# Kernel optimization log

Hardware: AMD Instinct MI355X
Metric: run time of the kernel (lower is better)

The kernel has to match this reference:

```python
import jax, jax.numpy as jnp
import numpy as np

B, D, H, O, E = 1048576, 17, 8, 6, 4  # batch, input_dim, expert_hidden, output_dim, n_clusters
G1, G2 = 64, 32  # gating hidden dims


def setup_inputs() -> dict:
    key = jax.random.key(0)
    ks = jax.random.split(key, 14)
    def w(k, shape, fan_in):
        return (jax.random.normal(k, shape, jnp.float32) / jnp.sqrt(jnp.float32(fan_in)))
    return {
        "x": jax.random.normal(ks[0], (B, D), jnp.float32),
        # per-expert MLP params, stacked on leading expert axis E
        "eW1": w(ks[1], (E, D, H), D), "eb1": w(ks[2], (E, H), D),
        "eW2": w(ks[3], (E, H, H), H), "eb2": w(ks[4], (E, H), H),
        "eW3": w(ks[5], (E, H, O), H), "eb3": w(ks[6], (E, O), H),
        # gating classifier params
        "gW1": w(ks[7], (D, G1), D), "gb1": w(ks[8], (G1,), D),
        "gW2": w(ks[9], (G1, G2), G1), "gb2": w(ks[10], (G2,), G1),
        "gW3": w(ks[11], (G2, E), G2), "gb3": w(ks[12], (E,), G2),
    }


def reference(x, eW1, eb1, eW2, eb2, eW3, eb3, gW1, gb1, gW2, gb2, gW3, gb3):
    # gating network: 17 -> 64 -> 32 -> 4 logits
    h = jax.nn.relu(x @ gW1 + gb1)
    h = jax.nn.relu(h @ gW2 + gb2)
    gating_logits = h @ gW3 + gb3  # [B, E]
    selected = jnp.argmax(gating_logits, axis=1)  # [B] hard routing
    # all experts computed (as in the original), stacked over expert axis
    e = jax.nn.relu(jnp.einsum('bi,eih->beh', x, eW1) + eb1)   # [B, E, H]
    e = jax.nn.relu(jnp.einsum('beh,ehk->bek', e, eW2) + eb2)  # [B, E, H]
    eo = jnp.einsum('bek,eko->beo', e, eW3) + eb3              # [B, E, O]
    # gather the selected expert's output per sample
    predictions = jnp.take_along_axis(eo, selected[:, None, None], axis=1)[:, 0, :]  # [B, O]
    return predictions, gating_logits
```

## Files before the change

### kernel.cpp

```cpp
#include <hip/hip_runtime.h>

#define BTOT 1048576
#define D 17
#define H 8
#define OUT 6
#define E 4
#define G1 64
#define G2 32
#define CHUNKS 4
#define XSTR 20

typedef float f32x4 __attribute__((ext_vector_type(4)));
typedef float f32x2 __attribute__((ext_vector_type(2)));
typedef short s16x8 __attribute__((ext_vector_type(8)));
typedef unsigned int uint;
typedef unsigned short ushort_t;

union U4S8 { uint u[4]; s16x8 s; };

__device__ __forceinline__ uint bfr(uint u) {
    return (u + 0x7fffu + ((u >> 16) & 1u)) & 0xffff0000u;
}

__device__ __forceinline__ void split1(float v, uint &h, uint &m, uint &l) {
    uint hb = bfr(__float_as_uint(v));
    float r1 = v - __uint_as_float(hb);
    uint mb = bfr(__float_as_uint(r1));
    float r2 = r1 - __uint_as_float(mb);
    uint lb = bfr(__float_as_uint(r2));
    h = hb >> 16; m = mb >> 16; l = lb >> 16;
}

__device__ __forceinline__ void split_pair(float a, float b, uint &hp, uint &mp, uint &lp) {
    uint ha = bfr(__float_as_uint(a));
    uint hb = bfr(__float_as_uint(b));
    hp = (ha >> 16) | hb;
    float ra = a - __uint_as_float(ha);
    float rb = b - __uint_as_float(hb);
    uint ma = bfr(__float_as_uint(ra));
    uint mb = bfr(__float_as_uint(rb));
    mp = (ma >> 16) | mb;
    float sa = ra - __uint_as_float(ma);
    float sb = rb - __uint_as_float(mb);
    lp = (bfr(__float_as_uint(sa)) >> 16) | bfr(__float_as_uint(sb));
}

__device__ __forceinline__ void split8(f32x4 va, f32x4 vb, s16x8 &fh, s16x8 &fm, s16x8 &fl) {
    U4S8 Hh, Mm, Ll;
    split_pair(va.x, va.y, Hh.u[0], Mm.u[0], Ll.u[0]);
    split_pair(va.z, va.w, Hh.u[1], Mm.u[1], Ll.u[1]);
    split_pair(vb.x, vb.y, Hh.u[2], Mm.u[2], Ll.u[2]);
    split_pair(vb.z, vb.w, Hh.u[3], Mm.u[3], Ll.u[3]);
    fh = Hh.s; fm = Mm.s; fl = Ll.s;
}

#define MM6(dacc, ah, am, al, bh, bm, bl)                                        \
    dacc = __builtin_amdgcn_mfma_f32_16x16x32_bf16(al, bh, dacc, 0, 0, 0);       \
    dacc = __builtin_amdgcn_mfma_f32_16x16x32_bf16(am, bm, dacc, 0, 0, 0);       \
    dacc = __builtin_amdgcn_mfma_f32_16x16x32_bf16(ah, bl, dacc, 0, 0, 0);       \
    dacc = __builtin_amdgcn_mfma_f32_16x16x32_bf16(am, bh, dacc, 0, 0, 0);       \
    dacc = __builtin_amdgcn_mfma_f32_16x16x32_bf16(ah, bm, dacc, 0, 0, 0);       \
    dacc = __builtin_amdgcn_mfma_f32_16x16x32_bf16(ah, bh, dacc, 0, 0, 0);

#define WSTR 296

__global__ __launch_bounds__(256, 2) void hybrid_ruc_kernel(
    const float* __restrict__ x,
    const float* __restrict__ eW1, const float* __restrict__ eb1,
    const float* __restrict__ eW2, const float* __restrict__ eb2,
    const float* __restrict__ eW3, const float* __restrict__ eb3,
    const float* __restrict__ gW1, const float* __restrict__ gb1,
    const float* __restrict__ gW2, const float* __restrict__ gb2,
    const float* __restrict__ gW3, const float* __restrict__ gb3,
    float* __restrict__ out)
{
    __shared__ __align__(16) float    sxp[256 * XSTR];
    __shared__ __align__(16) ushort_t sW1[3][64 * 24];
    __shared__ __align__(16) ushort_t sW2[3][32 * 72];
    __shared__ __align__(16) ushort_t sW3[3][4 * 32];
    __shared__ __align__(16) float    sscr[4][1024];
    __shared__ __align__(16) float    swl[E * WSTR];

    const int tid = threadIdx.x;
    const int wv  = tid >> 6;
    const int ln  = tid & 63;
    const int g   = ln >> 4;
    const int nn  = ln & 15;
    float* scr = sscr[wv];

    for (int t = tid; t < 64 * 24; t += 256) {
        int n = t / 24, k = t % 24;
        float v = (k < D) ? gW1[k * G1 + n] : 0.0f;
        uint h, m, l; split1(v, h, m, l);
        sW1[0][t] = (ushort_t)h; sW1[1][t] = (ushort_t)m; sW1[2][t] = (ushort_t)l;
    }
    for (int t = tid; t < 32 * 64; t += 256) {
        int n = t >> 6, k = t & 63;
        uint h, m, l; split1(gW2[k * G2 + n], h, m, l);
        int a = n * 72 + k;
        sW2[0][a] = (ushort_t)h; sW2[1][a] = (ushort_t)m; sW2[2][a] = (ushort_t)l;
    }
    if (tid < 4 * 32) {
        int n = tid >> 5, k = tid & 31;
        uint h, m, l; split1(gW3[k * E + n], h, m, l);
        int a = n * 32 + k;
        sW3[0][a] = (ushort_t)h; sW3[1][a] = (ushort_t)m; sW3[2][a] = (ushort_t)l;
    }
    for (int t = tid; t < E * D * H; t += 256) {
        swl[(t / 136) * WSTR + (t % 136)] = eW1[t];
    }
    if (tid < E * H * H) {
        swl[(tid / 64) * WSTR + 144 + (tid % 64)] = eW2[tid];
    }
    if (tid < E * H * OUT) {
        int e = tid / 48, r = tid % 48, k = r / 6, o = r % 6;
        swl[e * WSTR + 216 + k * 8 + o] = eW3[tid];
    }
    if (tid < E * H) swl[(tid / 8) * WSTR + 136 + (tid % 8)] = eb1[tid];
    if (tid < E * H) swl[(tid / 8) * WSTR + 208 + (tid % 8)] = eb2[tid];
    if (tid < E * OUT) swl[(tid / 6) * WSTR + 280 + (tid % 6)] = eb3[tid];
    __syncthreads();

    float cb1[4], cb2[2], cb3;
    #pragma unroll
    for (int ct = 0; ct < 4; ++ct) cb1[ct] = gb1[ct * 16 + nn];
    cb2[0] = gb2[nn]; cb2[1] = gb2[16 + nn];
    cb3 = (nn < 4) ? gb3[nn] : 0.0f;

    const s16x8 z8 = {0, 0, 0, 0, 0, 0, 0, 0};
    s16x8 B1f[3][4];
    #pragma unroll
    for (int kd = 0; kd < 3; ++kd)
        #pragma unroll
        for (int ct = 0; ct < 4; ++ct)
            B1f[kd][ct] = (g <= 2) ? *(const s16x8*)(&sW1[kd][(ct * 16 + nn) * 24 + g * 8]) : z8;
    s16x8 B2f[3][2][2];
    #pragma unroll
    for (int kd = 0; kd < 3; ++kd)
        #pragma unroll
        for (int ct = 0; ct < 2; ++ct)
            #pragma unroll
            for (int kt = 0; kt < 2; ++kt)
                B2f[kd][ct][kt] = *(const s16x8*)(&sW2[kd][(ct * 16 + nn) * 72 + kt * 32 + g * 8]);
    s16x8 B3f[3];
    #pragma unroll
    for (int kd = 0; kd < 3; ++kd)
        B3f[kd] = (nn < 4) ? *(const s16x8*)(&sW3[kd][nn * 32 + g * 8]) : z8;

    #pragma unroll 1
    for (int c = 0; c < CHUNKS; ++c) {
        if (c) __syncthreads();
        const long long cbase = ((long long)blockIdx.x * CHUNKS + c) * 256;

        for (int t = tid; t < 256 * D; t += 256) {
            int s = t / D, k = t % D;
            sxp[s * XSTR + k] = x[cbase * D + t];
        }
        {
            int s = tid;
            sxp[s * XSTR + 17] = 0.0f;
            sxp[s * XSTR + 18] = 0.0f;
            sxp[s * XSTR + 19] = 0.0f;
        }
        __syncthreads();

        f32x4 Lg[4];
        const f32x4 z4 = {0.0f, 0.0f, 0.0f, 0.0f};
        #pragma unroll
        for (int rt = 0; rt < 4; ++rt) {
            const int srow = wv * 64 + rt * 16 + nn;
            f32x4 xa = (g <= 2) ? *(const f32x4*)(&sxp[srow * XSTR + g * 8]) : z4;
            f32x4 xb = (g <= 1) ? *(const f32x4*)(&sxp[srow * XSTR + g * 8 + 4]) : z4;
            s16x8 a1h, a1m, a1l; split8(xa, xb, a1h, a1m, a1l);

            #pragma unroll
            for (int ct = 0; ct < 4; ++ct) {
                f32x4 d = {cb1[ct], cb1[ct], cb1[ct], cb1[ct]};
                MM6(d, a1h, a1m, a1l, B1f[0][ct], B1f[1][ct], B1f[2][ct]);
                #pragma unroll
                for (int r = 0; r < 4; ++r) {
                    float hv = fmaxf(d[r], 0.0f);
                    int s = g * 4 + r, n = ct * 16 + nn;
                    scr[s * 64 + (((n >> 2) ^ (s & 15)) << 2) + (n & 3)] = hv;
                }
            }

            s16x8 a2h[2], a2m[2], a2l[2];
            #pragma unroll
            for (int kt = 0; kt < 2; ++kt) {
                int kb0 = kt * 8 + g * 2;
                f32x4 va = *(const f32x4*)(&scr[nn * 64 + ((kb0 ^ (nn & 15)) << 2)]);
                f32x4 vb = *(const f32x4*)(&scr[nn * 64 + (((kb0 + 1) ^ (nn & 15)) << 2)]);
                split8(va, vb, a2h[kt], a2m[kt], a2l[kt]);
            }

            #pragma unroll
            for (int ct = 0; ct < 2; ++ct) {
                f32x4 d = {cb2[ct], cb2[ct], cb2[ct], cb2[ct]};
                #pragma unroll
                for (int kt = 0; kt < 2; ++kt) {
                    MM6(d, a2h[kt], a2m[kt], a2l[kt], B2f[0][ct][kt], B2f[1][ct][kt], B2f[2][ct][kt]);
                }
                #pragma unroll
                for (int r = 0; r < 4; ++r) {
                    float hv = fmaxf(d[r], 0.0f);
                    int s = g * 4 + r, n = ct * 16 + nn;
                    scr[s * 32 + (((n >> 2) ^ (s & 7)) << 2) + (n & 3)] = hv;
                }
            }

            s16x8 a3h, a3m, a3l;
            {
                f32x4 va = *(const f32x4*)(&scr[nn * 32 + (((2 * g) ^ (nn & 7)) << 2)]);
                f32x4 vb = *(const f32x4*)(&scr[nn * 32 + (((2 * g + 1) ^ (nn & 7)) << 2)]);
                split8(va, vb, a3h, a3m, a3l);
            }
            f32x4 d3 = {cb3, cb3, cb3, cb3};
            MM6(d3, a3h, a3m, a3l, B3f[0], B3f[1], B3f[2]);
            Lg[rt] = d3;
        }

        if (nn < 4) {
            #pragma unroll
            for (int rt = 0; rt < 4; ++rt)
                #pragma unroll
                for (int r = 0; r < 4; ++r)
                    scr[(rt * 16 + g * 4 + r) * 4 + nn] = Lg[rt][r];
        }
        f32x4 lgv = *(const f32x4*)(&scr[ln * 4]);

        int sel = 0; float best = lgv.x;
        if (lgv.y > best) { best = lgv.y; sel = 1; }
        if (lgv.z > best) { best = lgv.z; sel = 2; }
        if (lgv.w > best) { best = lgv.w; sel = 3; }

        const float* xrow = &sxp[tid * XSTR];
        float xr[D];
        {
            f32x4 x0 = *(const f32x4*)(xrow);
            f32x4 x1 = *(const f32x4*)(xrow + 4);
            f32x4 x2 = *(const f32x4*)(xrow + 8);
            f32x4 x3 = *(const f32x4*)(xrow + 12);
            xr[0]=x0.x; xr[1]=x0.y; xr[2]=x0.z; xr[3]=x0.w;
            xr[4]=x1.x; xr[5]=x1.y; xr[6]=x1.z; xr[7]=x1.w;
            xr[8]=x2.x; xr[9]=x2.y; xr[10]=x2.z; xr[11]=x2.w;
            xr[12]=x3.x; xr[13]=x3.y; xr[14]=x3.z; xr[15]=x3.w;
            xr[16]=xrow[16];
        }
        const float* wl = &swl[sel * WSTR];

        float t1[H];
        {
            f32x4 ba = *(const f32x4*)(wl + 136);
            f32x4 bb = *(const f32x4*)(wl + 140);
            t1[0]=ba.x; t1[1]=ba.y; t1[2]=ba.z; t1[3]=ba.w;
            t1[4]=bb.x; t1[5]=bb.y; t1[6]=bb.z; t1[7]=bb.w;
        }
        #pragma unroll
        for (int i = 0; i < D; ++i) {
            const float xi = xr[i];
            f32x4 wa = *(const f32x4*)(wl + i * 8);
            f32x4 wb = *(const f32x4*)(wl + i * 8 + 4);
            t1[0] = __builtin_fmaf(xi, wa.x, t1[0]);
            t1[1] = __builtin_fmaf(xi, wa.y, t1[1]);
            t1[2] = __builtin_fmaf(xi, wa.z, t1[2]);
            t1[3] = __builtin_fmaf(xi, wa.w, t1[3]);
            t1[4] = __builtin_fmaf(xi, wb.x, t1[4]);
            t1[5] = __builtin_fmaf(xi, wb.y, t1[5]);
            t1[6] = __builtin_fmaf(xi, wb.z, t1[6]);
            t1[7] = __builtin_fmaf(xi, wb.w, t1[7]);
        }
        float t2[H];
        {
            f32x4 ba = *(const f32x4*)(wl + 208);
            f32x4 bb = *(const f32x4*)(wl + 212);
            t2[0]=ba.x; t2[1]=ba.y; t2[2]=ba.z; t2[3]=ba.w;
            t2[4]=bb.x; t2[5]=bb.y; t2[6]=bb.z; t2[7]=bb.w;
        }
        #pragma unroll
        for (int k = 0; k < H; ++k) {
            const float tv = fmaxf(t1[k], 0.0f);
            f32x4 wa = *(const f32x4*)(wl + 144 + k * 8);
            f32x4 wb = *(const f32x4*)(wl + 144 + k * 8 + 4);
            t2[0] = __builtin_fmaf(tv, wa.x, t2[0]);
            t2[1] = __builtin_fmaf(tv, wa.y, t2[1]);
            t2[2] = __builtin_fmaf(tv, wa.z, t2[2]);
            t2[3] = __builtin_fmaf(tv, wa.w, t2[3]);
            t2[4] = __builtin_fmaf(tv, wb.x, t2[4]);
            t2[5] = __builtin_fmaf(tv, wb.y, t2[5]);
            t2[6] = __builtin_fmaf(tv, wb.z, t2[6]);
            t2[7] = __builtin_fmaf(tv, wb.w, t2[7]);
        }
        float pred[OUT];
        {
            f32x4 ba = *(const f32x4*)(wl + 280);
            pred[0]=ba.x; pred[1]=ba.y; pred[2]=ba.z; pred[3]=ba.w;
            pred[4]=wl[284]; pred[5]=wl[285];
        }
        #pragma unroll
        for (int k = 0; k < H; ++k) {
            const float tv = fmaxf(t2[k], 0.0f);
            f32x4 wa = *(const f32x4*)(wl + 216 + k * 8);
            f32x2 wb = *(const f32x2*)(wl + 216 + k * 8 + 4);
            pred[0] = __builtin_fmaf(tv, wa.x, pred[0]);
            pred[1] = __builtin_fmaf(tv, wa.y, pred[1]);
            pred[2] = __builtin_fmaf(tv, wa.z, pred[2]);
            pred[3] = __builtin_fmaf(tv, wa.w, pred[3]);
            pred[4] = __builtin_fmaf(tv, wb.x, pred[4]);
            pred[5] = __builtin_fmaf(tv, wb.y, pred[5]);
        }

        const long long b = cbase + tid;
        f32x2 p0 = {pred[0], pred[1]};
        f32x2 p1 = {pred[2], pred[3]};
        f32x2 p2 = {pred[4], pred[5]};
        *(f32x2*)(out + b * 6)     = p0;
        *(f32x2*)(out + b * 6 + 2) = p1;
        *(f32x2*)(out + b * 6 + 4) = p2;
        float* lout = out + (long long)BTOT * OUT;
        *(f32x4*)(lout + b * 4) = lgv;
    }
}

extern "C" void kernel_launch(void* const* d_in, const int* in_sizes, int n_in,
                              void* d_out, int out_size, void* d_ws, size_t ws_size,
                              hipStream_t stream) {
    const float* x   = (const float*)d_in[0];
    const float* eW1 = (const float*)d_in[1];
    const float* eb1 = (const float*)d_in[2];
    const float* eW2 = (const float*)d_in[3];
    const float* eb2 = (const float*)d_in[4];
    const float* eW3 = (const float*)d_in[5];
    const float* eb3 = (const float*)d_in[6];
    const float* gW1 = (const float*)d_in[7];
    const float* gb1 = (const float*)d_in[8];
    const float* gW2 = (const float*)d_in[9];
    const float* gb2 = (const float*)d_in[10];
    const float* gW3 = (const float*)d_in[11];
    const float* gb3 = (const float*)d_in[12];
    float* out = (float*)d_out;

    dim3 grid(BTOT / (256 * CHUNKS)), block(256);
    hipLaunchKernelGGL(hybrid_ruc_kernel, grid, block, 0, stream,
                       x, eW1, eb1, eW2, eb2, eW3, eb3,
                       gW1, gb1, gW2, gb2, gW3, gb3, out);
}
```

Before: 224.0 us.

## Cut gating MFMA split to 5 terms with exact fp32 fallback for near ties

Weights are now split into two bf16 parts (hi/lo) instead of three, and activations use cheaper truncation-based three-way splits built with perm. This drops the per-tile MFMA count from six to five and reduces the shared-memory and register footprint. Rows whose top two gating logits fall within a small threshold are recomputed exactly in fp32 by the whole wave, so argmax routing stays correct. Other changes: x is staged unpadded (stride 17) with coalesced loads, and launch bounds allow three blocks per CU. The fallback adds divergent serial work whenever near-ties occur.

```diff
diff --git a/kernel.cpp b/kernel.cpp
--- a/kernel.cpp
+++ b/kernel.cpp
@@ -8,7 +8,8 @@
 #define G1 64
 #define G2 32
 #define CHUNKS 4
-#define XSTR 20
+#define XSTR 17
+#define GTHR 5.0e-3f
 
 typedef float f32x4 __attribute__((ext_vector_type(4)));
 typedef float f32x2 __attribute__((ext_vector_type(2)));
@@ -22,49 +23,41 @@
     return (u + 0x7fffu + ((u >> 16) & 1u)) & 0xffff0000u;
 }
 
-__device__ __forceinline__ void split1(float v, uint &h, uint &m, uint &l) {
+__device__ __forceinline__ void wsplit(float v, uint &h, uint &l) {
     uint hb = bfr(__float_as_uint(v));
-    float r1 = v - __uint_as_float(hb);
-    uint mb = bfr(__float_as_uint(r1));
-    float r2 = r1 - __uint_as_float(mb);
-    uint lb = bfr(__float_as_uint(r2));
-    h = hb >> 16; m = mb >> 16; l = lb >> 16;
-}
-
-__device__ __forceinline__ void split_pair(float a, float b, uint &hp, uint &mp, uint &lp) {
-    uint ha = bfr(__float_as_uint(a));
-    uint hb = bfr(__float_as_uint(b));
-    hp = (ha >> 16) | hb;
-    float ra = a - __uint_as_float(ha);
-    float rb = b - __uint_as_float(hb);
-    uint ma = bfr(__float_as_uint(ra));
-    uint mb = bfr(__float_as_uint(rb));
-    mp = (ma >> 16) | mb;
-    float sa = ra - __uint_as_float(ma);
-    float sb = rb - __uint_as_float(mb);
-    lp = (bfr(__float_as_uint(sa)) >> 16) | bfr(__float_as_uint(sb));
-}
-
-__device__ __forceinline__ void split8(f32x4 va, f32x4 vb, s16x8 &fh, s16x8 &fm, s16x8 &fl) {
+    float r = v - __uint_as_float(hb);
+    h = hb >> 16;
+    l = bfr(__float_as_uint(r)) >> 16;
+}
+
+__device__ __forceinline__ void split8t(const float* p, s16x8 &fh, s16x8 &fm, s16x8 &fl) {
     U4S8 Hh, Mm, Ll;
-    split_pair(va.x, va.y, Hh.u[0], Mm.u[0], Ll.u[0]);
-    split_pair(va.z, va.w, Hh.u[1], Mm.u[1], Ll.u[1]);
-    split_pair(vb.x, vb.y, Hh.u[2], Mm.u[2], Ll.u[2]);
-    split_pair(vb.z, vb.w, Hh.u[3], Mm.u[3], Ll.u[3]);
+    #pragma unroll
+    for (int i = 0; i < 4; ++i) {
+        float a = p[2 * i], b = p[2 * i + 1];
+        uint ua = __float_as_uint(a), ub = __float_as_uint(b);
+        Hh.u[i] = __builtin_amdgcn_perm(ub, ua, 0x07060302u);
+        float ra = a - __uint_as_float(ua & 0xffff0000u);
+        float rb = b - __uint_as_float(ub & 0xffff0000u);
+        uint ura = __float_as_uint(ra), urb = __float_as_uint(rb);
+        Mm.u[i] = __builtin_amdgcn_perm(urb, ura, 0x07060302u);
+        float sa = ra - __uint_as_float(ura & 0xffff0000u);
+        float sb = rb - __uint_as_float(urb & 0xffff0000u);
+        Ll.u[i] = __builtin_amdgcn_perm(__float_as_uint(sb), __float_as_uint(sa), 0x07060302u);
+    }
     fh = Hh.s; fm = Mm.s; fl = Ll.s;
 }
 
-#define MM6(dacc, ah, am, al, bh, bm, bl)                                        \
+#define MM5(dacc, ah, am, al, bh, bl)                                            \
+    dacc = __builtin_amdgcn_mfma_f32_16x16x32_bf16(am, bl, dacc, 0, 0, 0);       \
     dacc = __builtin_amdgcn_mfma_f32_16x16x32_bf16(al, bh, dacc, 0, 0, 0);       \
-    dacc = __builtin_amdgcn_mfma_f32_16x16x32_bf16(am, bm, dacc, 0, 0, 0);       \
     dacc = __builtin_amdgcn_mfma_f32_16x16x32_bf16(ah, bl, dacc, 0, 0, 0);       \
     dacc = __builtin_amdgcn_mfma_f32_16x16x32_bf16(am, bh, dacc, 0, 0, 0);       \
-    dacc = __builtin_amdgcn_mfma_f32_16x16x32_bf16(ah, bm, dacc, 0, 0, 0);       \
     dacc = __builtin_amdgcn_mfma_f32_16x16x32_bf16(ah, bh, dacc, 0, 0, 0);
 
-#define WSTR 296
-
-__global__ __launch_bounds__(256, 2) void hybrid_ruc_kernel(
+#define WSTR 292
+
+__global__ __launch_bounds__(256, 3) void hybrid_ruc_kernel(
     const float* __restrict__ x,
     const float* __restrict__ eW1, const float* __restrict__ eb1,
     const float* __restrict__ eW2, const float* __restrict__ eb2,
@@ -74,10 +67,13 @@
     const float* __restrict__ gW3, const float* __restrict__ gb3,
     float* __restrict__ out)
 {
-    __shared__ __align__(16) float    sxp[256 * XSTR];
-    __shared__ __align__(16) ushort_t sW1[3][64 * 24];
-    __shared__ __align__(16) ushort_t sW2[3][32 * 72];
-    __shared__ __align__(16) ushort_t sW3[3][4 * 32];
+    __shared__ __align__(16) float    sxp[256 * XSTR + 16];
+    __shared__ __align__(16) ushort_t sW1h[64 * 24];
+    __shared__ __align__(16) ushort_t sW1l[64 * 24];
+    __shared__ __align__(16) ushort_t sW2h[32 * 72];
+    __shared__ __align__(16) ushort_t sW2l[32 * 72];
+    __shared__ __align__(16) ushort_t sW3h[4 * 32];
+    __shared__ __align__(16) ushort_t sW3l[4 * 32];
     __shared__ __align__(16) float    sscr[4][1024];
     __shared__ __align__(16) float    swl[E * WSTR];
 
@@ -88,23 +84,24 @@
     const int nn  = ln & 15;
     float* scr = sscr[wv];
 
+    if (tid < 16) sxp[256 * XSTR + tid] = 0.0f;
     for (int t = tid; t < 64 * 24; t += 256) {
         int n = t / 24, k = t % 24;
         float v = (k < D) ? gW1[k * G1 + n] : 0.0f;
-        uint h, m, l; split1(v, h, m, l);
-        sW1[0][t] = (ushort_t)h; sW1[1][t] = (ushort_t)m; sW1[2][t] = (ushort_t)l;
+        uint h, l; wsplit(v, h, l);
+        sW1h[t] = (ushort_t)h; sW1l[t] = (ushort_t)l;
     }
     for (int t = tid; t < 32 * 64; t += 256) {
         int n = t >> 6, k = t & 63;
-        uint h, m, l; split1(gW2[k * G2 + n], h, m, l);
+        uint h, l; wsplit(gW2[k * G2 + n], h, l);
         int a = n * 72 + k;
-        sW2[0][a] = (ushort_t)h; sW2[1][a] = (ushort_t)m; sW2[2][a] = (ushort_t)l;
+        sW2h[a] = (ushort_t)h; sW2l[a] = (ushort_t)l;
     }
     if (tid < 4 * 32) {
         int n = tid >> 5, k = tid & 31;
-        uint h, m, l; split1(gW3[k * E + n], h, m, l);
-        int a = n * 32 + k;
-        sW3[0][a] = (ushort_t)h; sW3[1][a] = (ushort_t)m; sW3[2][a] = (ushort_t)l;
+        uint h, l; wsplit(gW3[k * E + n], h, l);
+        sW3h[tid] = (ushort_t)h; sW3l[tid] = (ushort_t)l;
+        (void)n; (void)k;
     }
     for (int t = tid; t < E * D * H; t += 256) {
         swl[(t / 136) * WSTR + (t % 136)] = eW1[t];
@@ -128,55 +125,49 @@
     cb3 = (nn < 4) ? gb3[nn] : 0.0f;
 
     const s16x8 z8 = {0, 0, 0, 0, 0, 0, 0, 0};
-    s16x8 B1f[3][4];
+    s16x8 B1h[4], B1l[4];
     #pragma unroll
-    for (int kd = 0; kd < 3; ++kd)
-        #pragma unroll
-        for (int ct = 0; ct < 4; ++ct)
-            B1f[kd][ct] = (g <= 2) ? *(const s16x8*)(&sW1[kd][(ct * 16 + nn) * 24 + g * 8]) : z8;
-    s16x8 B2f[3][2][2];
+    for (int ct = 0; ct < 4; ++ct) {
+        B1h[ct] = (g <= 2) ? *(const s16x8*)(&sW1h[(ct * 16 + nn) * 24 + g * 8]) : z8;
+        B1l[ct] = (g <= 2) ? *(const s16x8*)(&sW1l[(ct * 16 + nn) * 24 + g * 8]) : z8;
+    }
+    s16x8 B2h[2][2], B2l[2][2];
     #pragma unroll
-    for (int kd = 0; kd < 3; ++kd)
-        #pragma unroll
-        for (int ct = 0; ct < 2; ++ct)
-            #pragma unroll
-            for (int kt = 0; kt < 2; ++kt)
-                B2f[kd][ct][kt] = *(const s16x8*)(&sW2[kd][(ct * 16 + nn) * 72 + kt * 32 + g * 8]);
-    s16x8 B3f[3];
-    #pragma unroll
-    for (int kd = 0; kd < 3; ++kd)
-        B3f[kd] = (nn < 4) ? *(const s16x8*)(&sW3[kd][nn * 32 + g * 8]) : z8;
+    for (int ct = 0; ct < 2; ++ct)
+        #pragma unroll
+        for (int kt = 0; kt < 2; ++kt) {
+            B2h[ct][kt] = *(const s16x8*)(&sW2h[(ct * 16 + nn) * 72 + kt * 32 + g * 8]);
+            B2l[ct][kt] = *(const s16x8*)(&sW2l[(ct * 16 + nn) * 72 + kt * 32 + g * 8]);
+        }
+    s16x8 B3h = (nn < 4) ? *(const s16x8*)(&sW3h[nn * 32 + g * 8]) : z8;
+    s16x8 B3l = (nn < 4) ? *(const s16x8*)(&sW3l[nn * 32 + g * 8]) : z8;
 
     #pragma unroll 1
     for (int c = 0; c < CHUNKS; ++c) {
         if (c) __syncthreads();
         const long long cbase = ((long long)blockIdx.x * CHUNKS + c) * 256;
 
-        for (int t = tid; t < 256 * D; t += 256) {
-            int s = t / D, k = t % D;
-            sxp[s * XSTR + k] = x[cbase * D + t];
-        }
-        {
-            int s = tid;
-            sxp[s * XSTR + 17] = 0.0f;
-            sxp[s * XSTR + 18] = 0.0f;
-            sxp[s * XSTR + 19] = 0.0f;
+        #pragma unroll
+        for (int k = 0; k < D; ++k) {
+            int t = tid + k * 256;
+            sxp[t] = x[cbase * D + t];
         }
         __syncthreads();
 
         f32x4 Lg[4];
-        const f32x4 z4 = {0.0f, 0.0f, 0.0f, 0.0f};
         #pragma unroll
         for (int rt = 0; rt < 4; ++rt) {
             const int srow = wv * 64 + rt * 16 + nn;
-            f32x4 xa = (g <= 2) ? *(const f32x4*)(&sxp[srow * XSTR + g * 8]) : z4;
-            f32x4 xb = (g <= 1) ? *(const f32x4*)(&sxp[srow * XSTR + g * 8 + 4]) : z4;
-            s16x8 a1h, a1m, a1l; split8(xa, xb, a1h, a1m, a1l);
+            float xv[8];
+            const int xb = srow * XSTR + g * 8;
+            #pragma unroll
+            for (int j = 0; j < 8; ++j) xv[j] = sxp[xb + j];
+            s16x8 a1h, a1m, a1l; split8t(xv, a1h, a1m, a1l);
 
             #pragma unroll
             for (int ct = 0; ct < 4; ++ct) {
                 f32x4 d = {cb1[ct], cb1[ct], cb1[ct], cb1[ct]};
-                MM6(d, a1h, a1m, a1l, B1f[0][ct], B1f[1][ct], B1f[2][ct]);
+                MM5(d, a1h, a1m, a1l, B1h[ct], B1l[ct]);
                 #pragma unroll
                 for (int r = 0; r < 4; ++r) {
                     float hv = fmaxf(d[r], 0.0f);
@@ -189,9 +180,10 @@
             #pragma unroll
             for (int kt = 0; kt < 2; ++kt) {
                 int kb0 = kt * 8 + g * 2;
-                f32x4 va = *(const f32x4*)(&scr[nn * 64 + ((kb0 ^ (nn & 15)) << 2)]);
-                f32x4 vb = *(const f32x4*)(&scr[nn * 64 + (((kb0 + 1) ^ (nn & 15)) << 2)]);
-                split8(va, vb, a2h[kt], a2m[kt], a2l[kt]);
+                float hv8[8];
+                *(f32x4*)&hv8[0] = *(const f32x4*)(&scr[nn * 64 + ((kb0 ^ (nn & 15)) << 2)]);
+                *(f32x4*)&hv8[4] = *(const f32x4*)(&scr[nn * 64 + (((kb0 + 1) ^ (nn & 15)) << 2)]);
+                split8t(hv8, a2h[kt], a2m[kt], a2l[kt]);
             }
 
             #pragma unroll
@@ -199,7 +191,7 @@
                 f32x4 d = {cb2[ct], cb2[ct], cb2[ct], cb2[ct]};
                 #pragma unroll
                 for (int kt = 0; kt < 2; ++kt) {
-                    MM6(d, a2h[kt], a2m[kt], a2l[kt], B2f[0][ct][kt], B2f[1][ct][kt], B2f[2][ct][kt]);
+                    MM5(d, a2h[kt], a2m[kt], a2l[kt], B2h[ct][kt], B2l[ct][kt]);
                 }
                 #pragma unroll
                 for (int r = 0; r < 4; ++r) {
@@ -209,14 +201,13 @@
                 }
             }
 
-            s16x8 a3h, a3m, a3l;
-            {
-                f32x4 va = *(const f32x4*)(&scr[nn * 32 + (((2 * g) ^ (nn & 7)) << 2)]);
-                f32x4 vb = *(const f32x4*)(&scr[nn * 32 + (((2 * g + 1) ^ (nn & 7)) << 2)]);
-                split8(va, vb, a3h, a3m, a3l);
-            }
+            float h28[8];
+            *(f32x4*)&h28[0] = *(const f32x4*)(&scr[nn * 32 + (((2 * g) ^ (nn & 7)) << 2)]);
+            *(f32x4*)&h28[4] = *(const f32x4*)(&scr[nn * 32 + (((2 * g + 1) ^ (nn & 7)) << 2)]);
+            s16x8 a3h, a3m, a3l; split8t(h28, a3h, a3m, a3l);
+
             f32x4 d3 = {cb3, cb3, cb3, cb3};
-            MM6(d3, a3h, a3m, a3l, B3f[0], B3f[1], B3f[2]);
+            MM5(d3, a3h, a3m, a3l, B3h, B3l);
             Lg[rt] = d3;
         }
 
@@ -229,23 +220,55 @@
         }
         f32x4 lgv = *(const f32x4*)(&scr[ln * 4]);
 
-        int sel = 0; float best = lgv.x;
-        if (lgv.y > best) { best = lgv.y; sel = 1; }
-        if (lgv.z > best) { best = lgv.z; sel = 2; }
-        if (lgv.w > best) { best = lgv.w; sel = 3; }
-
-        const float* xrow = &sxp[tid * XSTR];
+        int sel = 0;
+        {
+            float b = lgv.x;
+            if (lgv.y > b) { b = lgv.y; sel = 1; }
+            if (lgv.z > b) { b = lgv.z; sel = 2; }
+            if (lgv.w > b) { b = lgv.w; sel = 3; }
+        }
+        float mx01 = fmaxf(lgv.x, lgv.y), mn01 = fminf(lgv.x, lgv.y);
+        float mx23 = fmaxf(lgv.z, lgv.w), mn23 = fminf(lgv.z, lgv.w);
+        float best   = fmaxf(mx01, mx23);
+        float second = fmaxf(fminf(mx01, mx23), (mx01 >= mx23) ? mn01 : mn23);
+
+        unsigned long long fmask = __ballot(best - second < GTHR);
+        if (fmask) {
+            do {
+                int sl = (int)__builtin_ctzll(fmask);
+                fmask &= (fmask - 1);
+                const int fr = wv * 64 + sl;
+                float h1j = gb1[ln];
+                #pragma unroll 1
+                for (int i = 0; i < D; ++i)
+                    h1j = __builtin_fmaf(sxp[fr * XSTR + i], gW1[i * G1 + ln], h1j);
+                scr[ln] = fmaxf(h1j, 0.0f);
+                int j2 = ln & 31;
+                float h2j = gb2[j2];
+                #pragma unroll 4
+                for (int c2 = 0; c2 < G1; ++c2)
+                    h2j = __builtin_fmaf(scr[c2], gW2[c2 * G2 + j2], h2j);
+                scr[64 + j2] = fmaxf(h2j, 0.0f);
+                int e = ln & 3;
+                float lge = gb3[e];
+                #pragma unroll 4
+                for (int jj = 0; jj < G2; ++jj)
+                    lge = __builtin_fmaf(scr[64 + jj], gW3[jj * E + e], lge);
+                float l0 = __shfl(lge, 0), l1 = __shfl(lge, 1);
+                float l2 = __shfl(lge, 2), l3 = __shfl(lge, 3);
+                int s2 = 0; float bb = l0;
+                if (l1 > bb) { bb = l1; s2 = 1; }
+                if (l2 > bb) { bb = l2; s2 = 2; }
+                if (l3 > bb) { bb = l3; s2 = 3; }
+                if (ln == sl) sel = s2;
+            } while (fmask);
+        }
+
         float xr[D];
         {
-            f32x4 x0 = *(const f32x4*)(xrow);
-            f32x4 x1 = *(const f32x4*)(xrow + 4);
-            f32x4 x2 = *(const f32x4*)(xrow + 8);
-            f32x4 x3 = *(const f32x4*)(xrow + 12);
-            xr[0]=x0.x; xr[1]=x0.y; xr[2]=x0.z; xr[3]=x0.w;
-            xr[4]=x1.x; xr[5]=x1.y; xr[6]=x1.z; xr[7]=x1.w;
-            xr[8]=x2.x; xr[9]=x2.y; xr[10]=x2.z; xr[11]=x2.w;
-            xr[12]=x3.x; xr[13]=x3.y; xr[14]=x3.z; xr[15]=x3.w;
-            xr[16]=xrow[16];
+            const float* xrow = &sxp[tid * XSTR];
+            #pragma unroll
+            for (int i = 0; i < D; ++i) xr[i] = xrow[i];
         }
         const float* wl = &swl[sel * WSTR];
 
```

After: 563.1 us. 2.51x slower.
